# Kernel tuning notes

Measured on AMD Instinct MI355X. Metric: run time of the kernel, lower is better.

## Reference

```python
import jax, jax.numpy as jnp
import numpy as np

HOPS = 2
BN_EPS = 1e-5


def _glorot(key, shape):
    fan_in = shape[-2]
    bound = 1.0 / np.sqrt(fan_in)
    return jax.random.uniform(key, shape, jnp.float32, -bound, bound)


def setup_inputs() -> dict:
    key = jax.random.key(0)
    ks = jax.random.split(key, 12)
    n, e = 50000, 800000
    in_c, hid, out_c = 128, 96, 64
    x = jax.random.normal(ks[0], (n, in_c), jnp.float32)
    edge_index = jax.random.randint(ks[1], (2, e), 0, n, jnp.int32)
    # MixHopLayer 0: hops+1 linears in_c -> hid (stacked)
    conv0_W = _glorot(ks[2], (HOPS + 1, in_c, hid))
    conv0_b = jnp.zeros((HOPS + 1, hid), jnp.float32)
    # MixHopLayer 1: hops+1 linears hid*(hops+1) -> out_c
    conv1_W = _glorot(ks[3], (HOPS + 1, hid * (HOPS + 1), out_c))
    conv1_b = jnp.zeros((HOPS + 1, out_c), jnp.float32)
    # BatchNorm1d(hid*(hops+1)) eval-mode params/buffers
    w = hid * (HOPS + 1)
    bn_gamma = jnp.ones((w,), jnp.float32)
    bn_beta = jnp.zeros((w,), jnp.float32)
    bn_mean = 0.1 * jax.random.normal(ks[4], (w,), jnp.float32)
    bn_var = jnp.ones((w,), jnp.float32) + 0.1 * jax.random.uniform(ks[5], (w,))
    # final projection out_c*(hops+1) -> out_c
    fp_W = _glorot(ks[6], (out_c * (HOPS + 1), out_c))
    fp_b = jnp.zeros((out_c,), jnp.float32)
    return dict(x=x, edge_index=edge_index, conv0_W=conv0_W, conv0_b=conv0_b,
                conv1_W=conv1_W, conv1_b=conv1_b, bn_gamma=bn_gamma, bn_beta=bn_beta,
                bn_mean=bn_mean, bn_var=bn_var, fp_W=fp_W, fp_b=fp_b)


def _gcn_norm(edge_index, n):
    # PyG gcn_norm with add_self_loops=True, improved=False, symmetric norm.
    row, col = edge_index[0], edge_index[1]
    loop = jnp.arange(n, dtype=edge_index.dtype)
    row = jnp.concatenate([row, loop])
    col = jnp.concatenate([col, loop])
    deg = jax.ops.segment_sum(jnp.ones_like(col, jnp.float32), col, num_segments=n)
    dinv = jnp.where(deg > 0, jax.lax.rsqrt(deg), 0.0)
    w = dinv[row] * dinv[col]
    return row, col, w


def _spmm_adj_t(row, col, w, x, n):
    # adj_t = SparseTensor(row=col, col=row, value=w): out[col] += w * x[row]
    return jax.ops.segment_sum(w[:, None] * x[row], col, num_segments=n)


def _mixhop_layer(x, W, b, row, col, w, n):
    xs = [x @ W[0] + b[0]]
    for j in range(1, HOPS + 1):
        xj = x @ W[j] + b[j]
        for _ in range(j):
            xj = _spmm_adj_t(row, col, w, xj, n)
        xs.append(xj)
    return jnp.concatenate(xs, axis=1)


def reference(x, edge_index, conv0_W, conv0_b, conv1_W, conv1_b,
              bn_gamma, bn_beta, bn_mean, bn_var, fp_W, fp_b):
    n = x.shape[0]
    row, col, w = _gcn_norm(edge_index, n)
    h = _mixhop_layer(x, conv0_W, conv0_b, row, col, w, n)
    # BatchNorm1d (eval) + ReLU; dropout is identity in eval
    h = bn_gamma * (h - bn_mean) * jax.lax.rsqrt(bn_var + BN_EPS) + bn_beta
    h = jax.nn.relu(h)
    h = _mixhop_layer(h, conv1_W, conv1_b, row, col, w, n)
    return h @ fp_W + fp_b
```

## Files before the change

### kernel.cpp

```cpp
#include <hip/hip_runtime.h>

#define IN_C 128
#define HID 96
#define OUT_C 64
#define W0C 288
#define W1C 192
#define CAP 5120
#define EPB 1024

typedef __bf16 bf16x8v __attribute__((ext_vector_type(8)));
typedef float  f32x4v  __attribute__((ext_vector_type(4)));

__global__ void k_combo_prep(const float* __restrict__ x, __bf16* __restrict__ xb, int n8,
                             const float* __restrict__ W0, const float* __restrict__ W1,
                             const float* __restrict__ Wf,
                             const float* __restrict__ gamma, const float* __restrict__ beta,
                             const float* __restrict__ mean, const float* __restrict__ var,
                             __bf16* __restrict__ w0t, __bf16* __restrict__ w1t,
                             __bf16* __restrict__ wft,
                             float* __restrict__ scale, float* __restrict__ shift,
                             int* __restrict__ zp, int nz,
                             int CB, int PB) {
    int b = blockIdx.x;
    if (b < CB) {
        int i = b * 256 + threadIdx.x;
        if (i >= n8) return;
        bf16x8v o;
#pragma unroll
        for (int q = 0; q < 8; q++) o[q] = (__bf16)x[i * 8 + q];
        *(bf16x8v*)(xb + (size_t)i * 8) = o;
    } else if (b < CB + PB) {
        const int T0 = 3 * IN_C * HID;
        const int T1 = 3 * W0C * OUT_C;
        const int T2 = W1C * OUT_C;
        int i = (b - CB) * 256 + threadIdx.x;
        if (i < T0) {
            int kn = IN_C * HID;
            int j = i / kn, r = i % kn;
            int k = r / HID, nn = r % HID;
            w0t[(size_t)j * kn + (size_t)nn * IN_C + k] = (__bf16)W0[i];
        } else if (i < T0 + T1) {
            int ii = i - T0;
            int kn = W0C * OUT_C;
            int j = ii / kn, r = ii % kn;
            int k = r / OUT_C, nn = r % OUT_C;
            w1t[(size_t)j * kn + (size_t)nn * W0C + k] = (__bf16)W1[ii];
        } else if (i < T0 + T1 + T2) {
            int ii = i - T0 - T1;
            int k = ii / OUT_C, nn = ii % OUT_C;
            wft[(size_t)nn * W1C + k] = (__bf16)Wf[ii];
        } else if (i < T0 + T1 + T2 + W0C) {
            int ii = i - T0 - T1 - T2;
            float s = gamma[ii] * rsqrtf(var[ii] + 1e-5f);
            scale[ii] = s;
            shift[ii] = beta[ii] - mean[ii] * s;
        }
    } else {
        int i = (b - CB - PB) * 256 + threadIdx.x;
        if (i < nz) zp[i] = 0;
    }
}

__global__ __launch_bounds__(256) void k_mega0(
        const int* __restrict__ row, const int* __restrict__ col,
        int* __restrict__ bcur ,
        int2* __restrict__ binned, int e, int SB,
        const __bf16* __restrict__ xb, const __bf16* __restrict__ w0t ,
        const float* __restrict__ bias , __bf16* __restrict__ h,
        const float* __restrict__ scale, const float* __restrict__ shift, int M) {
    const int RS = 104;
    __shared__ __bf16 tile[128 * RS];
    int tid = threadIdx.x;
    if ((int)blockIdx.x < SB) {
        int* hist  = (int*)tile;
        int* basep = hist + 256;
        int e0 = blockIdx.x * EPB;
        int cnt = min(EPB, e - e0);
        hist[tid] = 0;
        __syncthreads();
        int rr[4], cc[4], rk[4];
#pragma unroll
        for (int k = 0; k < 4; k++) {
            int idx = tid + k * 256;
            if (idx < cnt) {
                rr[k] = row[e0 + idx];
                cc[k] = col[e0 + idx];
                rk[k] = atomicAdd(&hist[cc[k] >> 8], 1);
            }
        }
        __syncthreads();
        {
            int hv = hist[tid];
            if (hv > 0) basep[tid] = atomicAdd(&bcur[tid * 16], hv);
        }
        __syncthreads();
#pragma unroll
        for (int k = 0; k < 4; k++) {
            int idx = tid + k * 256;
            if (idx < cnt) {
                int b = cc[k] >> 8;
                int pos = basep[b] + rk[k];
                if (pos < CAP)
                    binned[(size_t)b * CAP + pos] = make_int2(rr[k], cc[k]);
            }
        }
        return;
    }
    int wave = tid >> 6, lane = tid & 63;
    int ln = lane & 15, quad = lane >> 4;
    int rowBase = (blockIdx.x - SB) * 128;
    int waveRow = wave * 16;
    f32x4v acc[2][6];
#pragma unroll
    for (int u = 0; u < 2; u++)
#pragma unroll
        for (int t = 0; t < 6; t++) acc[u][t] = (f32x4v){0.f, 0.f, 0.f, 0.f};
    const __bf16* arow0 = xb + (size_t)(rowBase + waveRow + ln) * IN_C + quad * 8;
    const __bf16* arow1 = arow0 + (size_t)64 * IN_C;
#pragma unroll
    for (int k = 0; k < 4; k++) {
        bf16x8v a0 = *(const bf16x8v*)(arow0 + k * 32);
        bf16x8v a1 = *(const bf16x8v*)(arow1 + k * 32);
#pragma unroll
        for (int c = 0; c < 6; c++) {
            bf16x8v b = *(const bf16x8v*)(w0t + (size_t)(c * 16 + ln) * IN_C + k * 32 + quad * 8);
            acc[0][c] = __builtin_amdgcn_mfma_f32_16x16x32_bf16(a0, b, acc[0][c], 0, 0, 0);
            acc[1][c] = __builtin_amdgcn_mfma_f32_16x16x32_bf16(a1, b, acc[1][c], 0, 0, 0);
        }
    }
#pragma unroll
    for (int u = 0; u < 2; u++)
#pragma unroll
        for (int r = 0; r < 4; r++) {
            int lr = u * 64 + waveRow + quad * 4 + r;
#pragma unroll
            for (int c = 0; c < 6; c++) {
                int col2 = c * 16 + ln;
                float v = acc[u][c][r] + bias[col2];
                v = fmaxf(v * scale[col2] + shift[col2], 0.f);
                tile[lr * RS + col2] = (__bf16)v;
            }
        }
    __syncthreads();
#pragma unroll
    for (int s = 0; s < 6; s++) {
        int idx = tid + s * 256;
        int r = idx / 12, c8 = idx % 12;
        int grow = rowBase + r;
        if (grow < M)
            *(bf16x8v*)(h + (size_t)grow * W0C + c8 * 8) =
                *(const bf16x8v*)(tile + r * RS + c8 * 8);
    }
}

__global__ void k_deg_scan(const int2* __restrict__ binned, const int* __restrict__ bcur,
                           int* __restrict__ counts, float* __restrict__ dinv,
                           int* __restrict__ bscan, int n, int nb) {
    __shared__ int s[256];
    int tid = threadIdx.x;
    if ((int)blockIdx.x == nb) {
        int v = (tid < nb) ? bcur[tid * 16] : 0;
        s[tid] = v;
        __syncthreads();
        for (int off = 1; off < 256; off <<= 1) {
            int t = (tid >= off) ? s[tid - off] : 0;
            __syncthreads();
            s[tid] += t;
            __syncthreads();
        }
        if (tid < nb) bscan[tid] = s[tid] - v;
        return;
    }
    s[tid] = 0;
    __syncthreads();
    int cnt = min(bcur[blockIdx.x * 16], CAP);
    const int2* bin = binned + (size_t)blockIdx.x * CAP;
    for (int t = tid; t < cnt; t += 256)
        atomicAdd(&s[bin[t].y & 255], 1);
    __syncthreads();
    int node = (blockIdx.x << 8) + tid;
    if (node < n) {
        int d = s[tid];
        counts[node] = d;
        dinv[node] = rsqrtf((float)(d + 1));
    }
}

__global__ __launch_bounds__(256) void k_bucket_sort(
        const int2* __restrict__ binned, const int* __restrict__ counts,
        const int* __restrict__ bcur, const int* __restrict__ bscan,
        const float* __restrict__ dinv,
        int2* __restrict__ csr, int* __restrict__ row_ptr,
        float* __restrict__ arow, int n) {
    __shared__ int   s_src[CAP];
    __shared__ int   s_col[CAP];
    __shared__ int   s_ofs[256];
    __shared__ int   lcur[256];
    __shared__ float s_a[256];
    int tid = threadIdx.x;
    int node0 = blockIdx.x << 8;
    int base = bscan[blockIdx.x];
    int cnt  = min(bcur[blockIdx.x * 16], CAP);
    const int2* bin = binned + (size_t)blockIdx.x * CAP;

    int node = node0 + tid;
    int cdeg = (node < n) ? counts[node] : 0;
    s_ofs[tid] = cdeg;
    __syncthreads();
    for (int o = 1; o < 256; o <<= 1) {
        int u = (tid >= o) ? s_ofs[tid - o] : 0;
        __syncthreads();
        s_ofs[tid] += u;
        __syncthreads();
    }
    int nodeOfs = s_ofs[tid] - cdeg;
    if (node < n) {
        row_ptr[node] = base + nodeOfs;
        if (node == n - 1) row_ptr[n] = base + nodeOfs + cdeg;
    }
    lcur[tid] = 0;
    __syncthreads();
    for (int t = tid; t < cnt; t += 256)
        atomicAdd(&lcur[bin[t].x >> 8], 1);
    __syncthreads();
    {
        int v = lcur[tid];
        s_ofs[tid] = v;
        __syncthreads();
        for (int o = 1; o < 256; o <<= 1) {
            int u = (tid >= o) ? s_ofs[tid - o] : 0;
            __syncthreads();
            s_ofs[tid] += u;
            __syncthreads();
        }
        lcur[tid] = s_ofs[tid] - v;
    }
    __syncthreads();
    for (int t = tid; t < cnt; t += 256) {
        int2 rc = bin[t];
        int pos = atomicAdd(&lcur[rc.x >> 8], 1);
        s_src[pos] = rc.x;
        s_col[pos] = rc.y;
    }
    __syncthreads();
    s_ofs[tid] = nodeOfs;
    lcur[tid] = 0;
    s_a[tid] = 0.f;
    __syncthreads();
    for (int t = tid; t < cnt; t += 256) {
        int r = s_src[t], c = s_col[t];
        int local = c - node0;
        int pos = s_ofs[local] + atomicAdd(&lcur[local], 1);
        float wv = dinv[r] * dinv[c];
        csr[base + pos] = make_int2(r, __float_as_int(wv));
        atomicAdd(&s_a[local], wv);
    }
    __syncthreads();
    if (node < n) {
        float d = dinv[node];
        arow[node] = s_a[tid] + d * d;
    }
}


__global__ __launch_bounds__(256) void k_mf_l0b(
        const __bf16* __restrict__ s1, const __bf16* __restrict__ w0t,
        const float* __restrict__ bias , const float* __restrict__ arow,
        __bf16* __restrict__ h, __bf16* __restrict__ tp,
        const float* __restrict__ scale, const float* __restrict__ shift, int M) {
    const int RS = 104;
    __shared__ __bf16 tile[64 * RS];
    int tid = threadIdx.x;
    int wave = tid >> 6, lane = tid & 63;
    int ln = lane & 15, quad = lane >> 4;
    int rowBase = blockIdx.x * 64;
    int waveRow = wave * 16;
    const __bf16* w1p = w0t + (size_t)1 * HID * IN_C;
    const __bf16* w2p = w0t + (size_t)2 * HID * IN_C;
    f32x4v acc[2][6];
#pragma unroll
    for (int j = 0; j < 2; j++)
#pragma unroll
        for (int t = 0; t < 6; t++) acc[j][t] = (f32x4v){0.f, 0.f, 0.f, 0.f};
    const __bf16* arow0 = s1 + (size_t)(rowBase + waveRow + ln) * IN_C + quad * 8;
#pragma unroll
    for (int k = 0; k < 4; k++) {
        bf16x8v a0 = *(const bf16x8v*)(arow0 + k * 32);
#pragma unroll
        for (int c = 0; c < 6; c++) {
            bf16x8v b1 = *(const bf16x8v*)(w1p + (size_t)(c * 16 + ln) * IN_C + k * 32 + quad * 8);
            bf16x8v b2 = *(const bf16x8v*)(w2p + (size_t)(c * 16 + ln) * IN_C + k * 32 + quad * 8);
            acc[0][c] = __builtin_amdgcn_mfma_f32_16x16x32_bf16(a0, b1, acc[0][c], 0, 0, 0);
            acc[1][c] = __builtin_amdgcn_mfma_f32_16x16x32_bf16(a0, b2, acc[1][c], 0, 0, 0);
        }
    }
    float avs[4];
#pragma unroll
    for (int r = 0; r < 4; r++)
        avs[r] = arow[rowBase + waveRow + quad * 4 + r];
#pragma unroll
    for (int jj = 0; jj < 2; jj++) {
        const float* bj = bias + (jj + 1) * HID;
#pragma unroll
        for (int r = 0; r < 4; r++) {
            int lr = waveRow + quad * 4 + r;
            float av = avs[r];
#pragma unroll
            for (int c = 0; c < 6; c++) {
                int col = c * 16 + ln;
                float v = acc[jj][c][r] + av * bj[col];
                if (jj == 0) v = fmaxf(v * scale[HID + col] + shift[HID + col], 0.f);
                tile[lr * RS + col] = (__bf16)v;
            }
        }
        __syncthreads();
#pragma unroll
        for (int s = 0; s < 3; s++) {
            int idx = tid + s * 256;
            int r = idx / 12, c8 = idx % 12;
            int grow = rowBase + r;
            if (grow < M) {
                __bf16* dst = (jj == 0) ? (h + (size_t)grow * W0C + HID)
                                        : (tp + (size_t)grow * HID);
                *(bf16x8v*)(dst + c8 * 8) = *(const bf16x8v*)(tile + r * RS + c8 * 8);
            }
        }
        __syncthreads();
    }
}

__global__ __launch_bounds__(256) void k_mf_l1m(
        const __bf16* __restrict__ hb, const __bf16* __restrict__ w1t ,
        const float* __restrict__ bias ,
        __bf16* __restrict__ g, __bf16* __restrict__ u12, int M) {
    const int RS = 72;
    __shared__ __bf16 tile[64 * RS];
    int tid = threadIdx.x;
    int wave = tid >> 6, lane = tid & 63;
    int ln = lane & 15, quad = lane >> 4;
    int rowBase = blockIdx.x * 64;
    int waveRow = wave * 16;
    f32x4v acc[3][4];
#pragma unroll
    for (int j = 0; j < 3; j++)
#pragma unroll
        for (int t = 0; t < 4; t++) acc[j][t] = (f32x4v){0.f, 0.f, 0.f, 0.f};
    const __bf16* arow0 = hb + (size_t)(rowBase + waveRow + ln) * W0C + quad * 8;
#pragma unroll
    for (int k = 0; k < 9; k++) {
        bf16x8v a0 = *(const bf16x8v*)(arow0 + k * 32);
#pragma unroll
        for (int c = 0; c < 4; c++) {
#pragma unroll
            for (int j = 0; j < 3; j++) {
                bf16x8v b = *(const bf16x8v*)(w1t + (size_t)j * OUT_C * W0C +
                                              (size_t)(c * 16 + ln) * W0C + k * 32 + quad * 8);
                acc[j][c] = __builtin_amdgcn_mfma_f32_16x16x32_bf16(a0, b, acc[j][c], 0, 0, 0);
            }
        }
    }
#pragma unroll
    for (int j = 0; j < 3; j++) {
        const float* bj = bias + j * OUT_C;
#pragma unroll
        for (int r = 0; r < 4; r++) {
            int lr = waveRow + quad * 4 + r;
#pragma unroll
            for (int c = 0; c < 4; c++) {
                int col = c * 16 + ln;
                tile[lr * RS + col] = (__bf16)(acc[j][c][r] + bj[col]);
            }
        }
        __syncthreads();
        __bf16* dst = (j == 0) ? g : u12;
        int ld = (j == 0) ? W1C : 128;
        int c0 = (j == 2) ? OUT_C : 0;
#pragma unroll
        for (int s = 0; s < 2; s++) {
            int idx = tid + s * 256;
            int r = idx / 8, c8 = idx % 8;
            int grow = rowBase + r;
            if (grow < M)
                *(bf16x8v*)(dst + (size_t)grow * ld + c0 + c8 * 8) =
                    *(const bf16x8v*)(tile + r * RS + c8 * 8);
        }
        __syncthreads();
    }
}

__global__ __launch_bounds__(256) void k_mf_fin(
        const __bf16* __restrict__ gb, const __bf16* __restrict__ wft ,
        const float* __restrict__ bias, float* __restrict__ out, int M) {
    const int RS = 68;
    __shared__ float tile[128 * RS];
    int tid = threadIdx.x;
    int wave = tid >> 6, lane = tid & 63;
    int ln = lane & 15, quad = lane >> 4;
    int rowBase = blockIdx.x * 128;
    int waveRow = wave * 16;
    f32x4v acc[2][4];
#pragma unroll
    for (int u = 0; u < 2; u++)
#pragma unroll
        for (int t = 0; t < 4; t++) acc[u][t] = (f32x4v){0.f, 0.f, 0.f, 0.f};
    const __bf16* arow0 = gb + (size_t)(rowBase + waveRow + ln) * W1C + quad * 8;
    const __bf16* arow1 = arow0 + (size_t)64 * W1C;
#pragma unroll
    for (int k = 0; k < 6; k++) {
        bf16x8v a0 = *(const bf16x8v*)(arow0 + k * 32);
        bf16x8v a1 = *(const bf16x8v*)(arow1 + k * 32);
#pragma unroll
        for (int c = 0; c < 4; c++) {
            bf16x8v b = *(const bf16x8v*)(wft + (size_t)(c * 16 + ln) * W1C + k * 32 + quad * 8);
            acc[0][c] = __builtin_amdgcn_mfma_f32_16x16x32_bf16(a0, b, acc[0][c], 0, 0, 0);
            acc[1][c] = __builtin_amdgcn_mfma_f32_16x16x32_bf16(a1, b, acc[1][c], 0, 0, 0);
        }
    }
#pragma unroll
    for (int u = 0; u < 2; u++)
#pragma unroll
        for (int r = 0; r < 4; r++) {
            int lr = u * 64 + waveRow + quad * 4 + r;
#pragma unroll
            for (int c = 0; c < 4; c++) {
                int col = c * 16 + ln;
                tile[lr * RS + col] = acc[u][c][r] + bias[col];
            }
        }
    __syncthreads();
#pragma unroll
    for (int s = 0; s < 8; s++) {
        int idx = tid + s * 256;
        int r = idx / 16, c4 = idx % 16;
        int grow = rowBase + r;
        if (grow < M)
            *(float4*)(out + (size_t)grow * OUT_C + c4 * 4) =
                *(const float4*)(tile + r * RS + c4 * 4);
    }
}

template <int C8, int NPB, bool BNRELU>
__global__ void k_spmm(const __bf16* __restrict__ xin, int ldx,
                       __bf16* __restrict__ xout, int ldo,
                       const int* __restrict__ row_ptr, const int* __restrict__ counts,
                       const int2* __restrict__ csr,
                       const float* __restrict__ dinv, int n,
                       const float* __restrict__ scale, const float* __restrict__ shift,
                       int chan0) {
    int c8 = threadIdx.x % C8;
    int nl = threadIdx.x / C8;
    int node = blockIdx.x * NPB + nl;
    if (node >= n) return;
    float di = dinv[node];
    float lw = di * di;
    float acc[8];
    {
        bf16x8v v = *(const bf16x8v*)(xin + (size_t)node * ldx + c8 * 8);
#pragma unroll
        for (int q = 0; q < 8; q++) acc[q] = lw * (float)v[q];
    }
    int start = row_ptr[node];
    int cnt = counts[node];
    int k = 0;
    for (; k + 4 <= cnt; k += 4) {
        int2 p0 = csr[start + k + 0], p1 = csr[start + k + 1];
        int2 p2 = csr[start + k + 2], p3 = csr[start + k + 3];
        float w0 = __int_as_float(p0.y), w1 = __int_as_float(p1.y);
        float w2 = __int_as_float(p2.y), w3 = __int_as_float(p3.y);
        bf16x8v v0 = *(const bf16x8v*)(xin + (size_t)p0.x * ldx + c8 * 8);
        bf16x8v v1 = *(const bf16x8v*)(xin + (size_t)p1.x * ldx + c8 * 8);
        bf16x8v v2 = *(const bf16x8v*)(xin + (size_t)p2.x * ldx + c8 * 8);
        bf16x8v v3 = *(const bf16x8v*)(xin + (size_t)p3.x * ldx + c8 * 8);
#pragma unroll
        for (int q = 0; q < 8; q++)
            acc[q] += w0 * (float)v0[q] + w1 * (float)v1[q] +
                      w2 * (float)v2[q] + w3 * (float)v3[q];
    }
    for (; k < cnt; k++) {
        int2 p = csr[start + k];
        float w = __int_as_float(p.y);
        bf16x8v xv = *(const bf16x8v*)(xin + (size_t)p.x * ldx + c8 * 8);
#pragma unroll
        for (int q = 0; q < 8; q++) acc[q] += w * (float)xv[q];
    }
    bf16x8v o;
#pragma unroll
    for (int q = 0; q < 8; q++) {
        float v = acc[q];
        if (BNRELU) {
            int ch = chan0 + c8 * 8 + q;
            v = fmaxf(v * scale[ch] + shift[ch], 0.f);
        }
        o[q] = (__bf16)v;
    }
    *(bf16x8v*)(xout + (size_t)node * ldo + c8 * 8) = o;
}

template <int C8, int SPLIT, int NPB, bool BNA, bool BNB>
__global__ void k_spmm2(const __bf16* __restrict__ xin, int ldx,
                        __bf16* __restrict__ dstA, int ldA, int chanA,
                        __bf16* __restrict__ dstB, int ldB, int chanB,
                        const int* __restrict__ row_ptr, const int* __restrict__ counts,
                        const int2* __restrict__ csr,
                        const float* __restrict__ dinv, int n,
                        const float* __restrict__ scale, const float* __restrict__ shift) {
    int c8 = threadIdx.x % C8;
    int nl = threadIdx.x / C8;
    int node = blockIdx.x * NPB + nl;
    if (node >= n) return;
    float di = dinv[node];
    float lw = di * di;
    float acc[8];
    {
        bf16x8v v = *(const bf16x8v*)(xin + (size_t)node * ldx + c8 * 8);
#pragma unroll
        for (int q = 0; q < 8; q++) acc[q] = lw * (float)v[q];
    }
    int start = row_ptr[node];
    int cnt = counts[node];
    int k = 0;
    for (; k + 4 <= cnt; k += 4) {
        int2 p0 = csr[start + k + 0], p1 = csr[start + k + 1];
        int2 p2 = csr[start + k + 2], p3 = csr[start + k + 3];
        float w0 = __int_as_float(p0.y), w1 = __int_as_float(p1.y);
        float w2 = __int_as_float(p2.y), w3 = __int_as_float(p3.y);
        bf16x8v v0 = *(const bf16x8v*)(xin + (size_t)p0.x * ldx + c8 * 8);
        bf16x8v v1 = *(const bf16x8v*)(xin + (size_t)p1.x * ldx + c8 * 8);
        bf16x8v v2 = *(const bf16x8v*)(xin + (size_t)p2.x * ldx + c8 * 8);
        bf16x8v v3 = *(const bf16x8v*)(xin + (size_t)p3.x * ldx + c8 * 8);
#pragma unroll
        for (int q = 0; q < 8; q++)
            acc[q] += w0 * (float)v0[q] + w1 * (float)v1[q] +
                      w2 * (float)v2[q] + w3 * (float)v3[q];
    }
    for (; k < cnt; k++) {
        int2 p = csr[start + k];
        float w = __int_as_float(p.y);
        bf16x8v xv = *(const bf16x8v*)(xin + (size_t)p.x * ldx + c8 * 8);
#pragma unroll
        for (int q = 0; q < 8; q++) acc[q] += w * (float)xv[q];
    }
    bool isA = c8 < SPLIT;
    __bf16* dst = isA ? dstA : dstB;
    int ld   = isA ? ldA : ldB;
    int lc8  = isA ? c8 : c8 - SPLIT;
    int chan = isA ? chanA : chanB;
    bool bn  = isA ? BNA : BNB;
    bf16x8v o;
#pragma unroll
    for (int q = 0; q < 8; q++) {
        float v = acc[q];
        if (bn) {
            int ch = chan + lc8 * 8 + q;
            v = fmaxf(v * scale[ch] + shift[ch], 0.f);
        }
        o[q] = (__bf16)v;
    }
    *(bf16x8v*)(dst + (size_t)node * ld + lc8 * 8) = o;
}


extern "C" void kernel_launch(void* const* d_in, const int* in_sizes, int n_in,
                              void* d_out, int out_size, void* d_ws, size_t ws_size,
                              hipStream_t stream) {
    const int n = in_sizes[0] / IN_C;
    const int e = in_sizes[1] / 2;

    const float* x    = (const float*)d_in[0];
    const int*   ei   = (const int*)d_in[1];
    const float* W0   = (const float*)d_in[2];
    const float* b0   = (const float*)d_in[3];
    const float* W1   = (const float*)d_in[4];
    const float* b1   = (const float*)d_in[5];
    const float* bn_g = (const float*)d_in[6];
    const float* bn_b = (const float*)d_in[7];
    const float* bn_m = (const float*)d_in[8];
    const float* bn_v = (const float*)d_in[9];
    const float* Wf   = (const float*)d_in[10];
    const float* bf   = (const float*)d_in[11];
    float* out = (float*)d_out;

    const int* e_row = ei;
    const int* e_col = ei + e;

    char* ws = (char*)d_ws;
    size_t off = 0;
    auto alloc = [&](size_t bytes) -> void* {
        void* p = ws + off;
        off += (bytes + 255) & ~(size_t)255;
        return p;
    };
    const int NP = n + 128;
    int nb = (n + 255) / 256;

    int*    counts  = (int*)alloc((size_t)(n + 256 * 16) * 4);
    int*    bcur    = counts + n;
    int*    row_ptr = (int*)alloc((size_t)(n + 1) * 4);
    int*    bscan   = (int*)alloc(256 * 4);
    float*  dinv    = (float*)alloc((size_t)n * 4);
    float*  arow    = (float*)alloc((size_t)NP * 4);
    int2*   binned  = (int2*)alloc((size_t)nb * CAP * 8);
    int2*   csr     = (int2*)alloc((size_t)e * 8);
    float*  bnscale = (float*)alloc(W0C * 4);
    float*  bnshift = (float*)alloc(W0C * 4);
    __bf16* xb  = (__bf16*)alloc((size_t)NP * IN_C * 2);
    __bf16* w0t = (__bf16*)alloc((size_t)3 * HID * IN_C * 2);
    __bf16* w1t = (__bf16*)alloc((size_t)3 * OUT_C * W0C * 2);
    __bf16* wft = (__bf16*)alloc((size_t)OUT_C * W1C * 2);
    __bf16* s1  = (__bf16*)alloc((size_t)NP * 128 * 2);
    __bf16* tp  = (__bf16*)alloc((size_t)NP * HID * 2);
    __bf16* h   = (__bf16*)alloc((size_t)NP * W0C * 2);
    __bf16* g   = (__bf16*)alloc((size_t)NP * W1C * 2);
    __bf16* u12 = s1;
    __bf16* up  = tp;

    int n8 = n * IN_C / 8;
    int nz = 256 * 16;
    int ptotal = 3 * IN_C * HID + 3 * W0C * OUT_C + W1C * OUT_C + W0C;
    int CB = (n8 + 255) / 256;
    int PB = (ptotal + 255) / 256;
    int ZB = (nz + 255) / 256;
    k_combo_prep<<<dim3(CB + PB + ZB), dim3(256), 0, stream>>>(
        x, xb, n8, W0, W1, Wf, bn_g, bn_b, bn_m, bn_v,
        w0t, w1t, wft, bnscale, bnshift, bcur, nz, CB, PB);

    int SB = (e + EPB - 1) / EPB;
    int GG = (n + 127) / 128;
    k_mega0<<<dim3(SB + GG), dim3(256), 0, stream>>>(
        e_row, e_col, bcur, binned, e, SB,
        xb, w0t, b0, h, bnscale, bnshift, n);

    k_deg_scan<<<dim3(nb + 1), dim3(256), 0, stream>>>(binned, bcur, counts, dinv,
                                                       bscan, n, nb);

    k_bucket_sort<<<dim3(nb), dim3(256), 0, stream>>>(binned, counts, bcur, bscan, dinv,
                                                      csr, row_ptr, arow, n);

    dim3 g64((n + 63) / 64);

    k_spmm<16, 16, false><<<dim3((n + 15) / 16), dim3(256), 0, stream>>>(
        xb, IN_C, s1, 128, row_ptr, counts, csr, dinv, n, nullptr, nullptr, 0);
    k_mf_l0b<<<g64, dim3(256), 0, stream>>>(s1, w0t, b0, arow, h, tp, bnscale, bnshift, n);
    k_spmm<12, 16, true><<<dim3((n + 15) / 16), dim3(192), 0, stream>>>(
        tp, HID, h + 2 * HID, W0C, row_ptr, counts, csr, dinv, n,
        bnscale, bnshift, 2 * HID);

    k_mf_l1m<<<g64, dim3(256), 0, stream>>>(h, w1t, b1, g, u12, n);

    k_spmm2<16, 8, 16, false, false><<<dim3((n + 15) / 16), dim3(256), 0, stream>>>(
        u12, 128, g + OUT_C, W1C, 0, up, OUT_C, 0,
        row_ptr, counts, csr, dinv, n, nullptr, nullptr);
    k_spmm<8, 32, false><<<dim3((n + 31) / 32), dim3(256), 0, stream>>>(
        up, OUT_C, g + 2 * OUT_C, W1C, row_ptr, counts, csr, dinv, n,
        nullptr, nullptr, 0);

    k_mf_fin<<<dim3((n + 127) / 128), dim3(256), 0, stream>>>(g, wft, bf, out, n);
}
```

Baseline: 321.4 us.

## Pack binned edges into one int and split SpMM passes into column halves

Binned edges are stored as a single 32-bit word (source<<8 | local column) instead of an int2. This halves the binning traffic and the shared memory used by the bucket sort. Every SpMM launch is now split into two narrower launches over column halves, with more nodes per block. This is meant to shrink the gathered working set per pass so it stays in cache, at the cost of reading the CSR structure twice. SpMM also derives the neighbour count from row_ptr differences instead of a separate counts array, and the fused spmm2 kernel is removed.

```diff
diff --git a/kernel.cpp b/kernel.cpp
--- a/kernel.cpp
+++ b/kernel.cpp
@@ -10,6 +10,7 @@
 
 typedef __bf16 bf16x8v __attribute__((ext_vector_type(8)));
 typedef float  f32x4v  __attribute__((ext_vector_type(4)));
+
 
 __global__ void k_combo_prep(const float* __restrict__ x, __bf16* __restrict__ xb, int n8,
                              const float* __restrict__ W0, const float* __restrict__ W1,
@@ -64,7 +65,7 @@
 __global__ __launch_bounds__(256) void k_mega0(
         const int* __restrict__ row, const int* __restrict__ col,
         int* __restrict__ bcur ,
-        int2* __restrict__ binned, int e, int SB,
+        int* __restrict__ binned, int e, int SB,
         const __bf16* __restrict__ xb, const __bf16* __restrict__ w0t ,
         const float* __restrict__ bias , __bf16* __restrict__ h,
         const float* __restrict__ scale, const float* __restrict__ shift, int M) {
@@ -101,7 +102,7 @@
                 int b = cc[k] >> 8;
                 int pos = basep[b] + rk[k];
                 if (pos < CAP)
-                    binned[(size_t)b * CAP + pos] = make_int2(rr[k], cc[k]);
+                    binned[(size_t)b * CAP + pos] = (rr[k] << 8) | (cc[k] & 255);
             }
         }
         return;
@@ -153,7 +154,7 @@
     }
 }
 
-__global__ void k_deg_scan(const int2* __restrict__ binned, const int* __restrict__ bcur,
+__global__ void k_deg_scan(const int* __restrict__ binned, const int* __restrict__ bcur,
                            int* __restrict__ counts, float* __restrict__ dinv,
                            int* __restrict__ bscan, int n, int nb) {
     __shared__ int s[256];
@@ -174,9 +175,9 @@
     s[tid] = 0;
     __syncthreads();
     int cnt = min(bcur[blockIdx.x * 16], CAP);
-    const int2* bin = binned + (size_t)blockIdx.x * CAP;
+    const int* bin = binned + (size_t)blockIdx.x * CAP;
     for (int t = tid; t < cnt; t += 256)
-        atomicAdd(&s[bin[t].y & 255], 1);
+        atomicAdd(&s[bin[t] & 255], 1);
     __syncthreads();
     int node = (blockIdx.x << 8) + tid;
     if (node < n) {
@@ -187,13 +188,12 @@
 }
 
 __global__ __launch_bounds__(256) void k_bucket_sort(
-        const int2* __restrict__ binned, const int* __restrict__ counts,
+        const int* __restrict__ binned, const int* __restrict__ counts,
         const int* __restrict__ bcur, const int* __restrict__ bscan,
         const float* __restrict__ dinv,
         int2* __restrict__ csr, int* __restrict__ row_ptr,
         float* __restrict__ arow, int n) {
-    __shared__ int   s_src[CAP];
-    __shared__ int   s_col[CAP];
+    __shared__ int   s_pack[CAP];
     __shared__ int   s_ofs[256];
     __shared__ int   lcur[256];
     __shared__ float s_a[256];
@@ -201,7 +201,7 @@
     int node0 = blockIdx.x << 8;
     int base = bscan[blockIdx.x];
     int cnt  = min(bcur[blockIdx.x * 16], CAP);
-    const int2* bin = binned + (size_t)blockIdx.x * CAP;
+    const int* bin = binned + (size_t)blockIdx.x * CAP;
 
     int node = node0 + tid;
     int cdeg = (node < n) ? counts[node] : 0;
@@ -221,7 +221,7 @@
     lcur[tid] = 0;
     __syncthreads();
     for (int t = tid; t < cnt; t += 256)
-        atomicAdd(&lcur[bin[t].x >> 8], 1);
+        atomicAdd(&lcur[bin[t] >> 16], 1);
     __syncthreads();
     {
         int v = lcur[tid];
@@ -237,10 +237,9 @@
     }
     __syncthreads();
     for (int t = tid; t < cnt; t += 256) {
-        int2 rc = bin[t];
-        int pos = atomicAdd(&lcur[rc.x >> 8], 1);
-        s_src[pos] = rc.x;
-        s_col[pos] = rc.y;
+        int p = bin[t];
+        int pos = atomicAdd(&lcur[p >> 16], 1);
+        s_pack[pos] = p;
     }
     __syncthreads();
     s_ofs[tid] = nodeOfs;
@@ -248,10 +247,11 @@
     s_a[tid] = 0.f;
     __syncthreads();
     for (int t = tid; t < cnt; t += 256) {
-        int r = s_src[t], c = s_col[t];
-        int local = c - node0;
+        int p = s_pack[t];
+        int r = p >> 8;
+        int local = p & 255;
         int pos = s_ofs[local] + atomicAdd(&lcur[local], 1);
-        float wv = dinv[r] * dinv[c];
+        float wv = dinv[r] * dinv[node0 + local];
         csr[base + pos] = make_int2(r, __float_as_int(wv));
         atomicAdd(&s_a[local], wv);
     }
@@ -442,7 +442,7 @@
 template <int C8, int NPB, bool BNRELU>
 __global__ void k_spmm(const __bf16* __restrict__ xin, int ldx,
                        __bf16* __restrict__ xout, int ldo,
-                       const int* __restrict__ row_ptr, const int* __restrict__ counts,
+                       const int* __restrict__ row_ptr,
                        const int2* __restrict__ csr,
                        const float* __restrict__ dinv, int n,
                        const float* __restrict__ scale, const float* __restrict__ shift,
@@ -460,7 +460,7 @@
         for (int q = 0; q < 8; q++) acc[q] = lw * (float)v[q];
     }
     int start = row_ptr[node];
-    int cnt = counts[node];
+    int cnt = row_ptr[node + 1] - start;
     int k = 0;
     for (; k + 4 <= cnt; k += 4) {
         int2 p0 = csr[start + k + 0], p1 = csr[start + k + 1];
@@ -494,69 +494,6 @@
         o[q] = (__bf16)v;
     }
     *(bf16x8v*)(xout + (size_t)node * ldo + c8 * 8) = o;
-}
-
-template <int C8, int SPLIT, int NPB, bool BNA, bool BNB>
-__global__ void k_spmm2(const __bf16* __restrict__ xin, int ldx,
-                        __bf16* __restrict__ dstA, int ldA, int chanA,
-                        __bf16* __restrict__ dstB, int ldB, int chanB,
-                        const int* __restrict__ row_ptr, const int* __restrict__ counts,
-                        const int2* __restrict__ csr,
-                        const float* __restrict__ dinv, int n,
-                        const float* __restrict__ scale, const float* __restrict__ shift) {
-    int c8 = threadIdx.x % C8;
-    int nl = threadIdx.x / C8;
-    int node = blockIdx.x * NPB + nl;
-    if (node >= n) return;
-    float di = dinv[node];
-    float lw = di * di;
-    float acc[8];
-    {
-        bf16x8v v = *(const bf16x8v*)(xin + (size_t)node * ldx + c8 * 8);
-#pragma unroll
-        for (int q = 0; q < 8; q++) acc[q] = lw * (float)v[q];
-    }
-    int start = row_ptr[node];
-    int cnt = counts[node];
-    int k = 0;
-    for (; k + 4 <= cnt; k += 4) {
-        int2 p0 = csr[start + k + 0], p1 = csr[start + k + 1];
-        int2 p2 = csr[start + k + 2], p3 = csr[start + k + 3];
-        float w0 = __int_as_float(p0.y), w1 = __int_as_float(p1.y);
-        float w2 = __int_as_float(p2.y), w3 = __int_as_float(p3.y);
-        bf16x8v v0 = *(const bf16x8v*)(xin + (size_t)p0.x * ldx + c8 * 8);
-        bf16x8v v1 = *(const bf16x8v*)(xin + (size_t)p1.x * ldx + c8 * 8);
-        bf16x8v v2 = *(const bf16x8v*)(xin + (size_t)p2.x * ldx + c8 * 8);
-        bf16x8v v3 = *(const bf16x8v*)(xin + (size_t)p3.x * ldx + c8 * 8);
-#pragma unroll
-        for (int q = 0; q < 8; q++)
-            acc[q] += w0 * (float)v0[q] + w1 * (float)v1[q] +
-                      w2 * (float)v2[q] + w3 * (float)v3[q];
-    }
-    for (; k < cnt; k++) {
-        int2 p = csr[start + k];
-        float w = __int_as_float(p.y);
-        bf16x8v xv = *(const bf16x8v*)(xin + (size_t)p.x * ldx + c8 * 8);
-#pragma unroll
-        for (int q = 0; q < 8; q++) acc[q] += w * (float)xv[q];
-    }
-    bool isA = c8 < SPLIT;
-    __bf16* dst = isA ? dstA : dstB;
-    int ld   = isA ? ldA : ldB;
-    int lc8  = isA ? c8 : c8 - SPLIT;
-    int chan = isA ? chanA : chanB;
-    bool bn  = isA ? BNA : BNB;
-    bf16x8v o;
-#pragma unroll
-    for (int q = 0; q < 8; q++) {
-        float v = acc[q];
-        if (bn) {
-            int ch = chan + lc8 * 8 + q;
-            v = fmaxf(v * scale[ch] + shift[ch], 0.f);
-        }
-        o[q] = (__bf16)v;
-    }
-    *(bf16x8v*)(dst + (size_t)node * ld + lc8 * 8) = o;
 }
 
 
@@ -599,7 +536,7 @@
     int*    bscan   = (int*)alloc(256 * 4);
     float*  dinv    = (float*)alloc((size_t)n * 4);
     float*  arow    = (float*)alloc((size_t)NP * 4);
-    int2*   binned  = (int2*)alloc((size_t)nb * CAP * 8);
+    int*    binned  = (int*)alloc((size_t)nb * CAP * 4);
     int2*   csr     = (int2*)alloc((size_t)e * 8);
     float*  bnscale = (float*)alloc(W0C * 4);
     float*  bnshift = (float*)alloc(W0C * 4);
@@ -637,21 +574,30 @@
                                                       csr, row_ptr, arow, n);
 
     dim3 g64((n + 63) / 64);
-
-    k_spmm<16, 16, false><<<dim3((n + 15) / 16), dim3(256), 0, stream>>>(
-        xb, IN_C, s1, 128, row_ptr, counts, csr, dinv, n, nullptr, nullptr, 0);
+    dim3 gs32((n + 31) / 32);
+    dim3 gs64((n + 63) / 64);
+
+    k_spmm<8, 32, false><<<gs32, dim3(256), 0, stream>>>(
+        xb, IN_C, s1, 128, row_ptr, csr, dinv, n, nullptr, nullptr, 0);
+    k_spmm<8, 32, false><<<gs32, dim3(256), 0, stream>>>(
+        xb + 64, IN_C, s1 + 64, 128, row_ptr, csr, dinv, n, nullptr, nullptr, 0);
     k_mf_l0b<<<g64, dim3(256), 0, stream>>>(s1, w0t, b0, arow, h, tp, bnscale, bnshift, n);
-    k_spmm<12, 16, true><<<dim3((n + 15) / 16), dim3(192), 0, stream>>>(
-        tp, HID, h + 2 * HID, W0C, row_ptr, counts, csr, dinv, n,
-        bnscale, bnshift, 2 * HID);
+    k_spmm<6, 32, true><<<gs32, dim3(192), 0, stream>>>(
+        tp, HID, h + 2 * HID, W0C, row_ptr, csr, dinv, n, bnscale, bnshift, 2 * HID);
+    k_spmm<6, 32, true><<<gs32, dim3(192), 0, stream>>>(
+        tp + 48, HID, h + 2 * HID + 48, W0C, row_ptr, csr, dinv, n,
+        bnscale, bnshift, 2 * HID + 48);
 
     k_mf_l1m<<<g64, dim3(256), 0, stream>>>(h, w1t, b1, g, u12, n);
 
-    k_spmm2<16, 8, 16, false, false><<<dim3((n + 15) / 16), dim3(256), 0, stream>>>(
-        u12, 128, g + OUT_C, W1C, 0, up, OUT_C, 0,
-        row_ptr, counts, csr, dinv, n, nullptr, nullptr);
-    k_spmm<8, 32, false><<<dim3((n + 31) / 32), dim3(256), 0, stream>>>(
-        up, OUT_C, g + 2 * OUT_C, W1C, row_ptr, counts, csr, dinv, n,
+    k_spmm<8, 32, false><<<gs32, dim3(256), 0, stream>>>(
+        u12, 128, g + OUT_C, W1C, row_ptr, csr, dinv, n, nullptr, nullptr, 0);
+    k_spmm<8, 32, false><<<gs32, dim3(256), 0, stream>>>(
+        u12 + 64, 128, up, OUT_C, row_ptr, csr, dinv, n, nullptr, nullptr, 0);
+    k_spmm<4, 64, false><<<gs64, dim3(256), 0, stream>>>(
+        up, OUT_C, g + 2 * OUT_C, W1C, row_ptr, csr, dinv, n, nullptr, nullptr, 0);
+    k_spmm<4, 64, false><<<gs64, dim3(256), 0, stream>>>(
+        up + 32, OUT_C, g + 2 * OUT_C + 32, W1C, row_ptr, csr, dinv, n,
         nullptr, nullptr, 0);
 
     k_mf_fin<<<dim3((n + 127) / 128), dim3(256), 0, stream>>>(g, wft, bf, out, n);
```

Measured after the change: 350.0 us. 1.09x slower.
